# Optimization experiments

Measured on AMD Instinct MI355X. Metric: run time of the kernel, lower is better.

## Reference

```python
import jax, jax.numpy as jnp
import numpy as np

B, T, C, H, HD = 2, 2048, 1024, 16, 64
EPS = 1e-6

def rmsnorm(x):
    return x * jax.lax.rsqrt(jnp.mean(x * x, axis=-1, keepdims=True) + EPS)

def rotary_cos_sin(seq_len, hd):
    inv_freq = 1.0 / (10000.0 ** (jnp.arange(0, hd, 2, dtype=jnp.float32) / hd))
    freqs = jnp.arange(seq_len, dtype=jnp.float32)[:, None] * inv_freq[None, :]  # [T, hd/2]
    return jnp.cos(freqs)[None, :, None, :], jnp.sin(freqs)[None, :, None, :]

def apply_rotary(x, cos, sin):
    x1, x2 = x[..., : HD // 2], x[..., HD // 2 :]
    return jnp.concatenate([x1 * cos + x2 * sin, -x1 * sin + x2 * cos], axis=-1)


def setup_inputs() -> dict:
    key = jax.random.key(0)
    ks = jax.random.split(key, 8)
    return {
        "x": jax.random.normal(ks[0], (B, T, C), jnp.float32),
        "w_qkv": jax.random.normal(ks[1], (3 * C, C), jnp.float32) * 0.02,
        "w_out": jax.random.normal(ks[2], (C, C), jnp.float32) * 0.02,
        "hyp_curvature": jax.random.uniform(ks[3], (1, H, 1, 1), jnp.float32, 0.5, 1.5),
        "w_uv": jax.random.normal(ks[4], (8 * C, C), jnp.float32) * 0.02,
        "b_uv": jnp.zeros((8 * C,), jnp.float32),
        "w_mlp_out": jax.random.normal(ks[5], (C, 4 * C), jnp.float32) * 0.02,
        "b_mlp_out": jnp.zeros((C,), jnp.float32),
    }


def reference(x, w_qkv, w_out, hyp_curvature, w_uv, b_uv, w_mlp_out, b_mlp_out):
    # --- pre-norm (euc/hyp branch uses rms_norm) ---
    h = rmsnorm(x)
    # --- QKV projection ---
    qkv = h @ w_qkv.T  # [B,T,3C]
    q, k, v = jnp.split(qkv, 3, axis=-1)
    q = q.reshape(B, T, H, HD)
    k = k.reshape(B, T, H, HD)
    v = v.reshape(B, T, H, HD)
    # --- RoPE ---
    cos, sin = rotary_cos_sin(T, HD)
    q = apply_rotary(q, cos, sin)
    k = apply_rotary(k, cos, sin)
    # [B,H,T,HD]
    q = jnp.transpose(q, (0, 2, 1, 3))
    k = jnp.transpose(k, (0, 2, 1, 3))
    v = jnp.transpose(v, (0, 2, 1, 3))
    # --- hyperbolic (Lorentz) attention ---
    kc = hyp_curvature  # [1,H,1,1], positive per-head curvature
    q0 = jnp.sqrt(kc + jnp.sum(q * q, axis=-1, keepdims=True))  # time coord [B,H,T,1]
    k0 = jnp.sqrt(kc + jnp.sum(k * k, axis=-1, keepdims=True))
    # Lorentz inner product <u,v>_L = -u0*v0 + u.v  -> [B,H,T,S]
    lorentz = jnp.einsum("bhtd,bhsd->bhts", q, k) - q0 * jnp.swapaxes(k0, -1, -2)
    dis = jnp.sqrt(kc) * jnp.arccosh(jnp.maximum(-lorentz / kc, 1.0 + EPS))
    causal = jnp.tril(jnp.ones((T, T), dtype=bool))
    scores = jnp.where(causal, -dis, -jnp.inf)  # hyp_attn_weight='neg_dis'
    attn_w = jax.nn.softmax(scores, axis=-1)
    attn = jnp.einsum("bhts,bhsd->bhtd", attn_w, v)
    attn = jnp.transpose(attn, (0, 2, 1, 3)).reshape(B, T, C)
    x = x + attn @ w_out.T
    # --- SwiGLU MLP with pre rms_norm ---
    h = rmsnorm(x)
    uv = h @ w_uv.T + b_uv
    u, vg = jnp.split(uv, 2, axis=-1)
    h_mlp = (u * jax.nn.silu(vg)) @ w_mlp_out.T + b_mlp_out
    return x + h_mlp
```

## Files before the change

kernel.cpp:

```cpp
#include <hip/hip_runtime.h>
#include <cstdint>
#include <cmath>

typedef __bf16 bf16;
typedef __attribute__((ext_vector_type(8))) __bf16 bf16x8;
typedef __attribute__((ext_vector_type(4))) __bf16 bf16x4;
typedef __attribute__((ext_vector_type(2))) __bf16 bf16x2;
typedef __attribute__((ext_vector_type(4))) float f32x4;

constexpr int B_ = 2, T_ = 2048, C_ = 1024, H_ = 16, HD_ = 64;
constexpr int M_ = B_ * T_;

#define EXP2F(x) __builtin_amdgcn_exp2f(x)
#define LOG2F(x) __builtin_amdgcn_logf(x)
#define SQRTF(x) __builtin_amdgcn_sqrtf(x)
#define RCPF(x)  __builtin_amdgcn_rcpf(x)

__device__ __forceinline__ void gld16(const void* g, void* l) {
  __builtin_amdgcn_global_load_lds((const __attribute__((address_space(1))) void*)g,
                                   (__attribute__((address_space(3))) void*)l, 16, 0, 0);
}

__global__ __launch_bounds__(256) void cast_all_kernel(const float* __restrict__ s0,
                                                       const float* __restrict__ s1,
                                                       const float* __restrict__ s2,
                                                       const float* __restrict__ s3,
                                                       const float* __restrict__ s4,
                                                       bf16* __restrict__ d0,
                                                       bf16* __restrict__ d1,
                                                       bf16* __restrict__ d2,
                                                       bf16* __restrict__ d3,
                                                       float* __restrict__ d4) {
  size_t gid = (size_t)blockIdx.x * 256 + threadIdx.x;
  if (gid >= 786432 + 262144 + 2097152 + 1048576) {
    size_t g4 = gid - (786432 + 262144 + 2097152 + 1048576);
    if (g4 >= 2048) return;
    int r = (int)(g4 * 4);
    int dr;
    if (r < 4096) { int g = r >> 5, i = r & 31; dr = g * 64 + i; }
    else { int j = r - 4096; int g = j >> 5, i = j & 31; dr = g * 64 + 32 + i; }
    *(f32x4*)(d4 + dr) = *(const f32x4*)(s4 + r);
    return;
  }
  const float* src;
  bf16* dst;
  size_t dstoff;
  if (gid < 786432) { src = s0; dst = d0; dstoff = gid * 4; }
  else if (gid < 786432 + 262144) { gid -= 786432; src = s1; dst = d1; dstoff = gid * 4; }
  else if (gid < 786432 + 262144 + 2097152) {
    gid -= 786432 + 262144; src = s2; dst = d2;
    size_t elem = gid * 4;
    int r = (int)(elem >> 10), c = (int)(elem & 1023);
    int dr;
    if (r < 4096) { int g = r >> 5, i = r & 31; dr = g * 64 + i; }
    else { int j = r - 4096; int g = j >> 5, i = j & 31; dr = g * 64 + 32 + i; }
    dstoff = ((size_t)dr << 10) | (size_t)c;
  }
  else { gid -= 786432 + 262144 + 2097152; src = s3; dst = d3; dstoff = gid * 4; }
  f32x4 v = *(const f32x4*)(src + gid * 4);
  bf16x4 o;
  o[0] = (bf16)v[0]; o[1] = (bf16)v[1]; o[2] = (bf16)v[2]; o[3] = (bf16)v[3];
  *(bf16x4*)(dst + dstoff) = o;
}

template <int MODE, typename OutT, int BM = 128>
__global__ __launch_bounds__(256) void gemm_bt(const bf16* __restrict__ A,
                                               const bf16* __restrict__ Bw,
                                               OutT* __restrict__ Cmat,
                                               const float* __restrict__ bias,
                                               const float* __restrict__ R,
                                               int M, int N, int K, int lda) {
  __shared__ __align__(16) bf16 shmem[(2 * BM + 2 * 128) * 32];
  bf16* const AlsH[2] = { &shmem[0], &shmem[BM * 32] };
  bf16* const BlsH[2] = { &shmem[2 * BM * 32], &shmem[2 * BM * 32 + 4096] };
  const int tid  = threadIdx.x;
  const int wave = tid >> 6;
  const int lane = tid & 63;
  const int quad = lane >> 4;
  const int l16  = lane & 15;
  const int bm = blockIdx.x * BM;
  const int bn = blockIdx.y * 128;
  const int wm = (wave & 1) * (BM / 2);
  const int wn = (wave >> 1) * 64;
  const int srow   = lane >> 2;
  const int schunk = lane & 3;
  constexpr int MT = BM / 32;

  f32x4 acc[MT][4];
#pragma unroll
  for (int i = 0; i < MT; i++)
#pragma unroll
    for (int j = 0; j < 4; j++) acc[i][j] = f32x4{0.f, 0.f, 0.f, 0.f};

  const bf16* Ag = A  + (size_t)(bm + wave * (BM / 4) + srow) * lda + schunk * 8;
  const bf16* Bg = Bw + (size_t)(bn + wave * 32 + srow) * K   + schunk * 8;
  bf16* AlsW0 = AlsH[0] + (wave * (BM / 4)) * 32;
  bf16* AlsW1 = AlsH[1] + (wave * (BM / 4)) * 32;
  bf16* BlsW0 = BlsH[0] + (wave * 32) * 32;
  bf16* BlsW1 = BlsH[1] + (wave * 32) * 32;

  for (int k0 = 0; k0 < K; k0 += 64) {
    gld16(Ag + k0, AlsW0);
    if (BM == 128) gld16(Ag + k0 + (size_t)16 * lda, AlsW0 + 16 * 32);
    gld16(Ag + k0 + 32, AlsW1);
    if (BM == 128) gld16(Ag + k0 + 32 + (size_t)16 * lda, AlsW1 + 16 * 32);
    gld16(Bg + k0,                       BlsW0);
    gld16(Bg + k0 + (size_t)16 * K,      BlsW0 + 16 * 32);
    gld16(Bg + k0 + 32,                  BlsW1);
    gld16(Bg + k0 + 32 + (size_t)16 * K, BlsW1 + 16 * 32);
    __syncthreads();

#pragma unroll
    for (int hh = 0; hh < 2; hh++) {
      bf16x8 af[MT], bfr[4];
#pragma unroll
      for (int mt = 0; mt < MT; mt++)
        af[mt] = *(const bf16x8*)&AlsH[hh][(wm + mt * 16 + l16) * 32 + quad * 8];
#pragma unroll
      for (int nt = 0; nt < 4; nt++)
        bfr[nt] = *(const bf16x8*)&BlsH[hh][(wn + nt * 16 + l16) * 32 + quad * 8];
#pragma unroll
      for (int mt = 0; mt < MT; mt++)
#pragma unroll
        for (int nt = 0; nt < 4; nt++)
          acc[mt][nt] = __builtin_amdgcn_mfma_f32_16x16x32_bf16(af[mt], bfr[nt], acc[mt][nt], 0, 0, 0);
    }
    __syncthreads();
  }

#pragma unroll
  for (int mt = 0; mt < MT; mt++) {
    const int row = bm + wm + mt * 16 + quad * 4;
#pragma unroll
    for (int nt = 0; nt < 4; nt++) {
      const int col = bn + wn + nt * 16 + l16;
      float bval = 0.f;
      if (MODE & 2) bval = bias[col];
#pragma unroll
      for (int r = 0; r < 4; r++) {
        float v = acc[mt][nt][r] + bval;
        if (MODE & 1) v += R[(size_t)(row + r) * N + col];
        Cmat[(size_t)(row + r) * N + col] = (OutT)v;
      }
    }
  }
}

__global__ __launch_bounds__(512, 2) void gemm8_swiglu(const bf16* __restrict__ A,
                                                       const bf16* __restrict__ Bw,
                                                       bf16* __restrict__ Cmat,
                                                       const float* __restrict__ bias) {
  constexpr int K = 1024, NTILE = K / 64;
  __shared__ __align__(16) bf16 smem[2][2][256][64];

  const int tid  = threadIdx.x;
  const int wave = tid >> 6, lane = tid & 63;
  const int quad = lane >> 4, l16 = lane & 15;
  const int wm = wave >> 2, wn = wave & 3;
  const int bm = blockIdx.x * 256;
  const int bn = blockIdx.y * 256;

  const int csw = (tid & 7) ^ ((tid >> 3) & 7);
  const bf16* gA = A  + (size_t)(bm + (tid >> 3)) * K + csw * 8;
  const bf16* gB = Bw + (size_t)(bn + (tid >> 3)) * K + csw * 8;
  const int wrow = wave * 8;

  const int r7 = l16 & 7;

  f32x4 acc[8][4];
#pragma unroll
  for (int i = 0; i < 8; i++)
#pragma unroll
    for (int j = 0; j < 4; j++) acc[i][j] = f32x4{0.f, 0.f, 0.f, 0.f};

#define STAGE8(buf_, tile_, h_) do {                                          \
    const int mat_ = (h_) >> 1;                                               \
    const int r0_  = ((h_) & 1) * 128;                                        \
    const bf16* s_ = (mat_ ? gB : gA) + (size_t)r0_ * K + (size_t)(tile_) * 64; \
    bf16* d_ = &smem[buf_][mat_][r0_ + wrow][0];                              \
    gld16(s_, d_);                                                            \
    gld16(s_ + (size_t)64 * K, d_ + 64 * 64);                                 \
  } while (0)
#define STAGE_ALL(buf_, tile_) do {                                           \
    STAGE8(buf_, tile_, 0); STAGE8(buf_, tile_, 1);                           \
    STAGE8(buf_, tile_, 2); STAGE8(buf_, tile_, 3); } while (0)

  STAGE_ALL(0, 0);
  STAGE_ALL(1, 1);
  asm volatile("s_waitcnt vmcnt(8)" ::: "memory");
  asm volatile("s_barrier" ::: "memory");

#pragma unroll 1
  for (int t = 0; t < NTILE; ++t) {
    const int buf = t & 1;
    bf16x8 afX[2][4], bfX[2][4];
#pragma unroll
    for (int nt = 0; nt < 4; nt++)
      bfX[0][nt] = *(const bf16x8*)&smem[buf][1][wn * 64 + nt * 16 + l16][(quad ^ r7) * 8];
#pragma unroll
    for (int i = 0; i < 4; i++)
      afX[0][i] = *(const bf16x8*)&smem[buf][0][wm * 128 + i * 16 + l16][(quad ^ r7) * 8];

#pragma unroll
    for (int ph = 0; ph < 4; ph++) {
      const int mh = ph & 1;
      const int ks = ph >> 1;
      if (ph == 0) {
#pragma unroll
        for (int i = 0; i < 4; i++)
          afX[1][i] = *(const bf16x8*)&smem[buf][0][wm * 128 + (4 + i) * 16 + l16][(quad ^ r7) * 8];
      } else if (ph == 1) {
#pragma unroll
        for (int nt = 0; nt < 4; nt++)
          bfX[1][nt] = *(const bf16x8*)&smem[buf][1][wn * 64 + nt * 16 + l16][((4 + quad) ^ r7) * 8];
#pragma unroll
        for (int i = 0; i < 4; i++)
          afX[0][i] = *(const bf16x8*)&smem[buf][0][wm * 128 + i * 16 + l16][((4 + quad) ^ r7) * 8];
      } else if (ph == 2) {
#pragma unroll
        for (int i = 0; i < 4; i++)
          afX[1][i] = *(const bf16x8*)&smem[buf][0][wm * 128 + (4 + i) * 16 + l16][((4 + quad) ^ r7) * 8];
      }
      __builtin_amdgcn_s_setprio(1);
#pragma unroll
      for (int i = 0; i < 4; i++)
#pragma unroll
        for (int nt = 0; nt < 4; nt++)
          acc[mh * 4 + i][nt] =
              __builtin_amdgcn_mfma_f32_16x16x32_bf16(afX[mh][i], bfX[ks][nt], acc[mh * 4 + i][nt], 0, 0, 0);
      __builtin_amdgcn_s_setprio(0);
    }

    if (t + 1 < NTILE) {
      asm volatile("s_barrier" ::: "memory");
      if (t + 2 < NTILE) {
        STAGE_ALL(buf, t + 2);
        asm volatile("s_waitcnt vmcnt(8)" ::: "memory");
      } else {
        asm volatile("s_waitcnt vmcnt(0)" ::: "memory");
      }
      asm volatile("s_barrier" ::: "memory");
    }
  }
#undef STAGE_ALL
#undef STAGE8

  const int cg = (bn >> 1) + wn * 32;
#pragma unroll
  for (int ntl = 0; ntl < 2; ntl++) {
    const float bu = bias[bn + wn * 64 + ntl * 16 + l16];
    const float bv = bias[bn + wn * 64 + 32 + ntl * 16 + l16];
    const int col = cg + ntl * 16 + l16;
#pragma unroll
    for (int mt = 0; mt < 8; mt++) {
      const int row = bm + wm * 128 + mt * 16 + quad * 4;
#pragma unroll
      for (int r = 0; r < 4; r++) {
        float u = acc[mt][ntl][r] + bu;
        float v = acc[mt][ntl + 2][r] + bv;
        float sig = RCPF(1.f + EXP2F(-v * 1.44269504f));
        Cmat[(size_t)(row + r) * 4096 + col] = (bf16)(u * v * sig);
      }
    }
  }
}

__global__ __launch_bounds__(256) void rmsnorm_kernel(const float* __restrict__ X,
                                                      bf16* __restrict__ O) {
  const int row = blockIdx.x;
  const int tid = threadIdx.x;
  const int wave = tid >> 6;
  f32x4 v = *(const f32x4*)(X + (size_t)row * C_ + tid * 4);
  float s = v[0] * v[0] + v[1] * v[1] + v[2] * v[2] + v[3] * v[3];
#pragma unroll
  for (int off = 32; off >= 1; off >>= 1) s += __shfl_xor(s, off);
  __shared__ float wsum[4];
  __shared__ float scale_sh;
  if ((tid & 63) == 0) wsum[wave] = s;
  __syncthreads();
  if (tid == 0)
    scale_sh = rsqrtf((wsum[0] + wsum[1] + wsum[2] + wsum[3]) * (1.f / (float)C_) + 1e-6f);
  __syncthreads();
  const float sc = scale_sh;
  bf16x4 o;
  o[0] = (bf16)(v[0] * sc); o[1] = (bf16)(v[1] * sc);
  o[2] = (bf16)(v[2] * sc); o[3] = (bf16)(v[3] * sc);
  *(bf16x4*)(O + (size_t)row * C_ + tid * 4) = o;
}

__global__ __launch_bounds__(256) void rotary_kernel(bf16* __restrict__ qkv,
                                                     const float* __restrict__ kcb,
                                                     float* __restrict__ q0b,
                                                     float* __restrict__ k0b) {
  const int wid  = blockIdx.x * 4 + (threadIdx.x >> 6);
  const int lane = threadIdx.x & 63;
  const int b = wid >> 15;
  const int rem = wid & 32767;
  const int t = rem >> 4;
  const int h = rem & 15;
  const int i = lane & 31;
  const float invf = expf(-((float)i / 32.f) * 9.210340371976184f);
  const float ang = (float)t * invf;
  const float cx = cosf(ang), sx = sinf(ang);
  const float kc = kcb[h];
  bf16* qp = qkv + (size_t)(b * T_ + t) * 3072 + h * 64;

#pragma unroll
  for (int which = 0; which < 2; which++) {
    bf16* p = qp + which * 1024;
    float x1 = (float)p[i];
    float x2 = (float)p[i + 32];
    float o = (lane < 32) ? (x1 * cx + x2 * sx) : (x2 * cx - x1 * sx);
    float ss = o * o;
#pragma unroll
    for (int off = 32; off >= 1; off >>= 1) ss += __shfl_xor(ss, off);
    p[lane] = (bf16)o;
    if (lane == 0) {
      float* dst = which == 0 ? q0b : k0b;
      dst[(size_t)(b * H_ + h) * T_ + t] = SQRTF(kc + ss);
    }
  }
}

__global__ __launch_bounds__(512) void attn_kernel(const bf16* __restrict__ qkv,
                                                   const float* __restrict__ q0b,
                                                   const float* __restrict__ k0b,
                                                   const float* __restrict__ kcb,
                                                   bf16* __restrict__ outp) {
  __shared__ __align__(16) bf16 Kls[2][64][72];
  __shared__ __align__(16) bf16 Vt[2][64][68];
  __shared__ __align__(16) bf16 Pls[8][16 * 36];
  __shared__ float k0s[2][64];

  const int tid = threadIdx.x;
  const int wave = tid >> 6, lane = tid & 63;
  const int quad = lane >> 4, l16 = lane & 15;
  const int bh = blockIdx.x;
  const int b = bh >> 4, h = bh & 15;

  const float kc = kcb[h];
  const float inv_kc = 1.f / kc;
  const float sqkc = SQRTF(kc);
  const int role = tid >> 8;
  const int st = tid & 255;
  const int sp = st & 31, dq = st >> 5;
  bf16* Pl = Pls[wave];
  const float* q0base = q0b + (size_t)(b * H_ + h) * T_;
  const float* k0base = k0b + (size_t)(b * H_ + h) * T_;

  const int yb = (int)blockIdx.y;
  const int ty = (yb < 8) ? (15 - yb) : (yb - 8);
  const int t0 = ty * 128;
  const int tb = t0 + wave * 16;
  const int nIter = 2 * ty + 2;

  const bf16* qrow = qkv + (size_t)(b * T_ + tb + l16) * 3072 + h * 64;
  bf16x8 aq0 = *(const bf16x8*)(qrow + quad * 8);
  bf16x8 aq1 = *(const bf16x8*)(qrow + 32 + quad * 8);
  float q0r[4];
#pragma unroll
  for (int r = 0; r < 4; r++) q0r[r] = q0base[tb + quad * 4 + r];

  f32x4 o[4];
#pragma unroll
  for (int dt = 0; dt < 4; dt++) o[dt] = f32x4{0.f, 0.f, 0.f, 0.f};
  float lrow[4] = {0.f, 0.f, 0.f, 0.f};

  const bf16* base = qkv + (size_t)b * T_ * 3072 + 1024 + role * 1024 + h * 64 + dq * 8;
  bf16x8 pf_a = *(const bf16x8*)(base + (size_t)(2 * sp) * 3072);
  bf16x8 pf_b = *(const bf16x8*)(base + (size_t)(2 * sp + 1) * 3072);
  float k0v = (tid < 64) ? k0base[tid] : 0.f;

  for (int it = 0; it < nIter; ++it) {
    const int s0 = it * 64;
    const int buf = it & 1;
    if (role == 0) {
      *(bf16x8*)&Kls[buf][2 * sp][dq * 8]     = pf_a;
      *(bf16x8*)&Kls[buf][2 * sp + 1][dq * 8] = pf_b;
    } else {
#pragma unroll
      for (int i2 = 0; i2 < 8; i2++) {
        bf16x2 pr;
        pr[0] = pf_a[i2];
        pr[1] = pf_b[i2];
        *(bf16x2*)&Vt[buf][dq * 8 + i2][2 * sp] = pr;
      }
    }
    if (tid < 64) k0s[buf][tid] = k0v;
    __syncthreads();

    const int s0n = (it + 1 < nIter) ? s0 + 64 : s0;
    pf_a = *(const bf16x8*)(base + (size_t)(s0n + 2 * sp) * 3072);
    pf_b = *(const bf16x8*)(base + (size_t)(s0n + 2 * sp + 1) * 3072);
    if (tid < 64) k0v = k0base[s0n + tid];

    if (s0 <= tb + 15) {
      f32x4 sc[4];
#pragma unroll
      for (int nt = 0; nt < 4; nt++) {
        sc[nt] = f32x4{0.f, 0.f, 0.f, 0.f};
        bf16x8 b0 = *(const bf16x8*)&Kls[buf][nt * 16 + l16][quad * 8];
        bf16x8 b1 = *(const bf16x8*)&Kls[buf][nt * 16 + l16][32 + quad * 8];
        sc[nt] = __builtin_amdgcn_mfma_f32_16x16x32_bf16(aq0, b0, sc[nt], 0, 0, 0);
        sc[nt] = __builtin_amdgcn_mfma_f32_16x16x32_bf16(aq1, b1, sc[nt], 0, 0, 0);
      }

      bf16x8 ap[2];
#pragma unroll
      for (int ck = 0; ck < 2; ck++) {
#pragma unroll
        for (int ntl = 0; ntl < 2; ntl++) {
          const int nt = ck * 2 + ntl;
          const float k0c = k0s[buf][nt * 16 + l16];
          const int s = s0 + nt * 16 + l16;
#pragma unroll
          for (int r = 0; r < 4; r++) {
            const int t = tb + quad * 4 + r;
            float lor = sc[nt][r] - q0r[r] * k0c;
            float ratio = fmaxf(-lor * inv_kc, 1.f + 1e-6f);
            float wv = ratio + SQRTF(ratio * ratio - 1.f);
            float p = EXP2F(-sqkc * LOG2F(wv));
            p = (s <= t) ? p : 0.f;
            lrow[r] += p;
            Pl[(quad * 4 + r) * 36 + ntl * 16 + l16] = (bf16)p;
          }
        }
        ap[ck] = *(const bf16x8*)&Pl[l16 * 36 + quad * 8];
      }
#pragma unroll
      for (int dt = 0; dt < 4; dt++) {
        bf16x8 bv0 = *(const bf16x8*)&Vt[buf][dt * 16 + l16][quad * 8];
        bf16x8 bv1 = *(const bf16x8*)&Vt[buf][dt * 16 + l16][32 + quad * 8];
        o[dt] = __builtin_amdgcn_mfma_f32_16x16x32_bf16(ap[0], bv0, o[dt], 0, 0, 0);
        o[dt] = __builtin_amdgcn_mfma_f32_16x16x32_bf16(ap[1], bv1, o[dt], 0, 0, 0);
      }
    }
  }

#pragma unroll
  for (int r = 0; r < 4; r++) {
#pragma unroll
    for (int off = 1; off <= 8; off <<= 1) lrow[r] += __shfl_xor(lrow[r], off);
  }
#pragma unroll
  for (int r = 0; r < 4; r++) {
    const float invl = RCPF(lrow[r]);
    const int t = tb + quad * 4 + r;
#pragma unroll
    for (int dt = 0; dt < 4; dt++) {
      float val = o[dt][r] * invl;
      outp[(size_t)(b * T_ + t) * C_ + h * 64 + dt * 16 + l16] = (bf16)val;
    }
  }
}

extern "C" void kernel_launch(void* const* d_in, const int* in_sizes, int n_in,
                              void* d_out, int out_size, void* d_ws, size_t ws_size,
                              hipStream_t stream) {
  const float* x      = (const float*)d_in[0];
  const float* w_qkv  = (const float*)d_in[1];
  const float* w_out  = (const float*)d_in[2];
  const float* kcb    = (const float*)d_in[3];
  const float* w_uv   = (const float*)d_in[4];
  const float* b_uv   = (const float*)d_in[5];
  const float* w_mlp  = (const float*)d_in[6];
  const float* b_mlp  = (const float*)d_in[7];
  float* out = (float*)d_out;

  const size_t MB = 1024ull * 1024ull;
  char* w = (char*)d_ws;
  bf16*  wqkv_b  = (bf16*)(w + 0);
  bf16*  wout_b  = (bf16*)(w + 6 * MB);
  bf16*  wuv_p   = (bf16*)(w + 8 * MB);
  bf16*  wmlp_b  = (bf16*)(w + 24 * MB);
  bf16*  hbuf    = (bf16*)(w + 32 * MB);
  bf16*  qkvbuf  = (bf16*)(w + 40 * MB);
  bf16*  attnbuf = (bf16*)(w + 64 * MB);
  bf16*  gbuf    = (bf16*)(w + 40 * MB);
  float* x2buf   = (float*)(w + 72 * MB);
  float* q0b     = (float*)(w + 88 * MB);
  float* k0b     = (float*)(w + 88 * MB + 256 * 1024);
  float* biasp   = (float*)(w + 88 * MB + 512 * 1024);

  const int total4 = 786432 + 262144 + 2097152 + 1048576 + 2048;
  cast_all_kernel<<<(total4 + 255) / 256, 256, 0, stream>>>(
      w_qkv, w_out, w_uv, w_mlp, b_uv, wqkv_b, wout_b, wuv_p, wmlp_b, biasp);

  rmsnorm_kernel<<<M_, 256, 0, stream>>>(x, hbuf);
  gemm_bt<0, bf16><<<dim3(M_ / 128, 3072 / 128), 256, 0, stream>>>(
      hbuf, wqkv_b, qkvbuf, nullptr, nullptr, M_, 3072, 1024, 1024);
  rotary_kernel<<<(B_ * T_ * H_) / 4, 256, 0, stream>>>(qkvbuf, kcb, q0b, k0b);
  attn_kernel<<<dim3(B_ * H_, 16), 512, 0, stream>>>(qkvbuf, q0b, k0b, kcb, attnbuf);
  gemm_bt<1, float, 64><<<dim3(M_ / 64, 1024 / 128), 256, 0, stream>>>(
      attnbuf, wout_b, x2buf, nullptr, x, M_, 1024, 1024, 1024);
  rmsnorm_kernel<<<M_, 256, 0, stream>>>(x2buf, hbuf);
  gemm8_swiglu<<<dim3(M_ / 256, 8192 / 256), 512, 0, stream>>>(hbuf, wuv_p, gbuf, biasp);
  gemm_bt<3, float, 64><<<dim3(M_ / 64, 1024 / 128), 256, 0, stream>>>(
      gbuf, wmlp_b, out, b_mlp, x2buf, M_, 1024, 4096, 4096);
}
```

Baseline: 384.4 us.

## Replace generic GEMM with double-buffered swizzled 128x128 pipeline kernel

```diff
diff --git a/kernel.cpp b/kernel.cpp
--- a/kernel.cpp
+++ b/kernel.cpp
@@ -63,77 +63,102 @@
   *(bf16x4*)(dst + dstoff) = o;
 }
 
-template <int MODE, typename OutT, int BM = 128>
-__global__ __launch_bounds__(256) void gemm_bt(const bf16* __restrict__ A,
-                                               const bf16* __restrict__ Bw,
-                                               OutT* __restrict__ Cmat,
-                                               const float* __restrict__ bias,
-                                               const float* __restrict__ R,
-                                               int M, int N, int K, int lda) {
-  __shared__ __align__(16) bf16 shmem[(2 * BM + 2 * 128) * 32];
-  bf16* const AlsH[2] = { &shmem[0], &shmem[BM * 32] };
-  bf16* const BlsH[2] = { &shmem[2 * BM * 32], &shmem[2 * BM * 32 + 4096] };
+template <int MODE, typename OutT>
+__global__ __launch_bounds__(256, 2) void gemm_fr(const bf16* __restrict__ A,
+                                                  const bf16* __restrict__ Bw,
+                                                  OutT* __restrict__ Cmat,
+                                                  const float* __restrict__ bias,
+                                                  const float* __restrict__ R,
+                                                  int N, int K) {
+  __shared__ __align__(16) bf16 smem[2][2][128][64];
+
   const int tid  = threadIdx.x;
-  const int wave = tid >> 6;
-  const int lane = tid & 63;
-  const int quad = lane >> 4;
-  const int l16  = lane & 15;
-  const int bm = blockIdx.x * BM;
+  const int wave = tid >> 6, lane = tid & 63;
+  const int quad = lane >> 4, l16 = lane & 15;
+  const int wm = wave >> 1, wn = wave & 1;
+  const int bm = blockIdx.x * 128;
   const int bn = blockIdx.y * 128;
-  const int wm = (wave & 1) * (BM / 2);
-  const int wn = (wave >> 1) * 64;
-  const int srow   = lane >> 2;
-  const int schunk = lane & 3;
-  constexpr int MT = BM / 32;
-
-  f32x4 acc[MT][4];
-#pragma unroll
-  for (int i = 0; i < MT; i++)
+
+  const int csw = (tid & 7) ^ ((tid >> 3) & 7);
+  const bf16* gA = A  + (size_t)(bm + (tid >> 3)) * K + csw * 8;
+  const bf16* gB = Bw + (size_t)(bn + (tid >> 3)) * K + csw * 8;
+  const int wrow = wave * 8;
+  const int r7 = l16 & 7;
+
+  f32x4 acc[4][4];
+#pragma unroll
+  for (int i = 0; i < 4; i++)
 #pragma unroll
     for (int j = 0; j < 4; j++) acc[i][j] = f32x4{0.f, 0.f, 0.f, 0.f};
 
-  const bf16* Ag = A  + (size_t)(bm + wave * (BM / 4) + srow) * lda + schunk * 8;
-  const bf16* Bg = Bw + (size_t)(bn + wave * 32 + srow) * K   + schunk * 8;
-  bf16* AlsW0 = AlsH[0] + (wave * (BM / 4)) * 32;
-  bf16* AlsW1 = AlsH[1] + (wave * (BM / 4)) * 32;
-  bf16* BlsW0 = BlsH[0] + (wave * 32) * 32;
-  bf16* BlsW1 = BlsH[1] + (wave * 32) * 32;
-
-  for (int k0 = 0; k0 < K; k0 += 64) {
-    gld16(Ag + k0, AlsW0);
-    if (BM == 128) gld16(Ag + k0 + (size_t)16 * lda, AlsW0 + 16 * 32);
-    gld16(Ag + k0 + 32, AlsW1);
-    if (BM == 128) gld16(Ag + k0 + 32 + (size_t)16 * lda, AlsW1 + 16 * 32);
-    gld16(Bg + k0,                       BlsW0);
-    gld16(Bg + k0 + (size_t)16 * K,      BlsW0 + 16 * 32);
-    gld16(Bg + k0 + 32,                  BlsW1);
-    gld16(Bg + k0 + 32 + (size_t)16 * K, BlsW1 + 16 * 32);
-    __syncthreads();
-
-#pragma unroll
-    for (int hh = 0; hh < 2; hh++) {
-      bf16x8 af[MT], bfr[4];
-#pragma unroll
-      for (int mt = 0; mt < MT; mt++)
-        af[mt] = *(const bf16x8*)&AlsH[hh][(wm + mt * 16 + l16) * 32 + quad * 8];
+#define STG(buf_, tile_, mat_, g_) do {                                        \
+    const bf16* s_ = (mat_ ? gB : gA) + (size_t)((g_) * 32) * K + (size_t)(tile_) * 64; \
+    gld16(s_, &smem[buf_][mat_][(g_) * 32 + wrow][0]);                         \
+  } while (0)
+#define STG_ALL(buf_, tile_) do {                                              \
+    STG(buf_, tile_, 0, 0); STG(buf_, tile_, 0, 1);                            \
+    STG(buf_, tile_, 0, 2); STG(buf_, tile_, 0, 3);                            \
+    STG(buf_, tile_, 1, 0); STG(buf_, tile_, 1, 1);                            \
+    STG(buf_, tile_, 1, 2); STG(buf_, tile_, 1, 3); } while (0)
+
+  const int NT = K >> 6;
+  STG_ALL(0, 0);
+  STG_ALL(1, 1);
+  asm volatile("s_waitcnt vmcnt(8)" ::: "memory");
+  asm volatile("s_barrier" ::: "memory");
+
+#pragma unroll 1
+  for (int t = 0; t < NT; ++t) {
+    const int buf = t & 1;
+    bf16x8 af[2][4], bfr[2][4];
+#pragma unroll
+    for (int nt = 0; nt < 4; nt++)
+      bfr[0][nt] = *(const bf16x8*)&smem[buf][1][wn * 64 + nt * 16 + l16][(quad ^ r7) * 8];
+#pragma unroll
+    for (int i = 0; i < 4; i++)
+      af[0][i] = *(const bf16x8*)&smem[buf][0][wm * 64 + i * 16 + l16][(quad ^ r7) * 8];
+#pragma unroll
+    for (int nt = 0; nt < 4; nt++)
+      bfr[1][nt] = *(const bf16x8*)&smem[buf][1][wn * 64 + nt * 16 + l16][((4 + quad) ^ r7) * 8];
+#pragma unroll
+    for (int i = 0; i < 4; i++)
+      af[1][i] = *(const bf16x8*)&smem[buf][0][wm * 64 + i * 16 + l16][((4 + quad) ^ r7) * 8];
+
+    __builtin_amdgcn_s_setprio(1);
+#pragma unroll
+    for (int i = 0; i < 4; i++)
 #pragma unroll
       for (int nt = 0; nt < 4; nt++)
-        bfr[nt] = *(const bf16x8*)&BlsH[hh][(wn + nt * 16 + l16) * 32 + quad * 8];
-#pragma unroll
-      for (int mt = 0; mt < MT; mt++)
-#pragma unroll
-        for (int nt = 0; nt < 4; nt++)
-          acc[mt][nt] = __builtin_amdgcn_mfma_f32_16x16x32_bf16(af[mt], bfr[nt], acc[mt][nt], 0, 0, 0);
-    }
-    __syncthreads();
-  }
-
-#pragma unroll
-  for (int mt = 0; mt < MT; mt++) {
-    const int row = bm + wm + mt * 16 + quad * 4;
+        acc[i][nt] = __builtin_amdgcn_mfma_f32_16x16x32_bf16(af[0][i], bfr[0][nt], acc[i][nt], 0, 0, 0);
+    __builtin_amdgcn_s_setprio(0);
+    __builtin_amdgcn_s_setprio(1);
+#pragma unroll
+    for (int i = 0; i < 4; i++)
+#pragma unroll
+      for (int nt = 0; nt < 4; nt++)
+        acc[i][nt] = __builtin_amdgcn_mfma_f32_16x16x32_bf16(af[1][i], bfr[1][nt], acc[i][nt], 0, 0, 0);
+    __builtin_amdgcn_s_setprio(0);
+
+    if (t + 1 < NT) {
+      asm volatile("s_barrier" ::: "memory");
+      if (t + 2 < NT) {
+        STG_ALL(buf, t + 2);
+        asm volatile("s_waitcnt vmcnt(8)" ::: "memory");
+      } else {
+        asm volatile("s_waitcnt vmcnt(0)" ::: "memory");
+      }
+      asm volatile("s_barrier" ::: "memory");
+    }
+  }
+#undef STG_ALL
+#undef STG
+
+#pragma unroll
+  for (int mt = 0; mt < 4; mt++) {
+    const int row = bm + wm * 64 + mt * 16 + quad * 4;
 #pragma unroll
     for (int nt = 0; nt < 4; nt++) {
-      const int col = bn + wn + nt * 16 + l16;
+      const int col = bn + wn * 64 + nt * 16 + l16;
       float bval = 0.f;
       if (MODE & 2) bval = bias[col];
 #pragma unroll
@@ -487,14 +512,14 @@
       w_qkv, w_out, w_uv, w_mlp, b_uv, wqkv_b, wout_b, wuv_p, wmlp_b, biasp);
 
   rmsnorm_kernel<<<M_, 256, 0, stream>>>(x, hbuf);
-  gemm_bt<0, bf16><<<dim3(M_ / 128, 3072 / 128), 256, 0, stream>>>(
-      hbuf, wqkv_b, qkvbuf, nullptr, nullptr, M_, 3072, 1024, 1024);
+  gemm_fr<0, bf16><<<dim3(M_ / 128, 3072 / 128), 256, 0, stream>>>(
+      hbuf, wqkv_b, qkvbuf, nullptr, nullptr, 3072, 1024);
   rotary_kernel<<<(B_ * T_ * H_) / 4, 256, 0, stream>>>(qkvbuf, kcb, q0b, k0b);
   attn_kernel<<<dim3(B_ * H_, 16), 512, 0, stream>>>(qkvbuf, q0b, k0b, kcb, attnbuf);
-  gemm_bt<1, float, 64><<<dim3(M_ / 64, 1024 / 128), 256, 0, stream>>>(
-      attnbuf, wout_b, x2buf, nullptr, x, M_, 1024, 1024, 1024);
+  gemm_fr<1, float><<<dim3(M_ / 128, 1024 / 128), 256, 0, stream>>>(
+      attnbuf, wout_b, x2buf, nullptr, x, 1024, 1024);
   rmsnorm_kernel<<<M_, 256, 0, stream>>>(x2buf, hbuf);
   gemm8_swiglu<<<dim3(M_ / 256, 8192 / 256), 512, 0, stream>>>(hbuf, wuv_p, gbuf, biasp);
-  gemm_bt<3, float, 64><<<dim3(M_ / 64, 1024 / 128), 256, 0, stream>>>(
-      gbuf, wmlp_b, out, b_mlp, x2buf, M_, 1024, 4096, 4096);
-}
+  gemm_fr<3, float><<<dim3(M_ / 128, 1024 / 128), 256, 0, stream>>>(
+      gbuf, wmlp_b, out, b_mlp, x2buf, 1024, 4096);
+}
```

After: 381.0 us. Within noise of the previous version (-0.9%).
